# Optimization experiments

Hardware: AMD Instinct MI355X
Metric: run time of the kernel (lower is better)

The kernel has to match this reference:

```python
import jax, jax.numpy as jnp
import numpy as np

BATCH = 16384
IN_F = 4096
OUT_F = 4096
CP_H = 4
CP_W = 4
CP_B = 4


def _cubic_interp_matrix(n_out: int, n_cp: int, a: float = -0.75) -> jnp.ndarray:
    """Dense (n_out, n_cp) matrix replicating torch bicubic interpolation
    (Keys cubic convolution, a=-0.75) along one axis with align_corners=True
    and border replication (index clamping)."""
    # source coordinate for each output index (align_corners=True)
    x = jnp.arange(n_out, dtype=jnp.float32) * ((n_cp - 1) / (n_out - 1))
    x0 = jnp.floor(x)
    t = x - x0                      # fractional offset in [0,1)
    x0i = x0.astype(jnp.int32)

    def cub_inner(s):   # |s| <= 1
        return ((a + 2.0) * s - (a + 3.0)) * s * s + 1.0

    def cub_outer(s):   # 1 < |s| < 2
        return ((a * s - 5.0 * a) * s + 8.0 * a) * s - 4.0 * a

    # weights for taps at offsets -1, 0, +1, +2
    ws = (cub_outer(t + 1.0), cub_inner(t), cub_inner(1.0 - t), cub_outer(2.0 - t))
    A = jnp.zeros((n_out, n_cp), dtype=jnp.float32)
    for k, w in enumerate(ws):
        idx = jnp.clip(x0i + (k - 1), 0, n_cp - 1)  # replicate border
        A = A + w[:, None] * jax.nn.one_hot(idx, n_cp, dtype=jnp.float32)
    return A


def _linear_interp_matrix(n_out: int, n_cp: int) -> jnp.ndarray:
    """Dense (n_out, n_cp) matrix replicating torch 1-D linear interpolation
    with align_corners=True."""
    x = jnp.arange(n_out, dtype=jnp.float32) * ((n_cp - 1) / (n_out - 1))
    lo = jnp.floor(x).astype(jnp.int32)
    t = x - lo.astype(jnp.float32)
    hi = jnp.clip(lo + 1, 0, n_cp - 1)
    oh = lambda i: jax.nn.one_hot(i, n_cp, dtype=jnp.float32)
    return (1.0 - t)[:, None] * oh(lo) + t[:, None] * oh(hi)


def setup_inputs() -> dict:
    key = jax.random.key(0)
    k1, k2, k3 = jax.random.split(key, 3)
    return {
        "x": jax.random.normal(k1, (BATCH, IN_F), dtype=jnp.float32),
        "weight_cp": jax.random.normal(k2, (CP_H, CP_W), dtype=jnp.float32) * 0.02,
        "bias_cp": jax.random.normal(k3, (CP_B,), dtype=jnp.float32) * 0.02,
    }


def reference(x, weight_cp, bias_cp):
    # Bicubic-interpolated dense weight: W = A_out @ CP @ A_in^T  (out, in)
    A_out = _cubic_interp_matrix(OUT_F, CP_H)
    A_in = _cubic_interp_matrix(IN_F, CP_W)
    W = A_out @ weight_cp @ A_in.T
    # Linearly interpolated bias (out,)
    bias = _linear_interp_matrix(OUT_F, CP_B) @ bias_cp
    # F.linear: y = x @ W^T + b
    return x @ W.T + bias
```

## Files before the change

kernel.cpp:

```cpp
#include <hip/hip_runtime.h>
#include <cstddef>

#define BATCH 16384
#define IN_F  4096
#define OUT_F 4096
#define ROWS_PER_BLOCK 4
#define NBLOCKS (BATCH / ROWS_PER_BLOCK)

__device__ __forceinline__ float cub_inner(float s) {
    return (1.25f * s - 2.25f) * s * s + 1.0f;
}
__device__ __forceinline__ float cub_outer(float s) {
    return ((-0.75f * s + 3.75f) * s - 6.0f) * s + 3.0f;
}

__device__ __forceinline__ void cubic_row(int i, float& a0, float& a1, float& a2, float& a3) {
    const float inv = 3.0f / 4095.0f;
    const float xi = (float)i * inv;
    const float x0 = floorf(xi);
    const float t  = xi - x0;
    const int   c  = (int)x0;
    const float w0 = cub_outer(t + 1.0f);
    const float w1 = cub_inner(t);
    const float w2 = cub_inner(1.0f - t);
    const float w3 = cub_outer(2.0f - t);
    if (c == 0)      { a0 = w0 + w1; a1 = w2;   a2 = w3;   a3 = 0.0f; }
    else if (c == 1) { a0 = w0;      a1 = w1;   a2 = w2;   a3 = w3; }
    else if (c == 2) { a0 = 0.0f;    a1 = w0;   a2 = w1;   a3 = w2 + w3; }
    else             { a0 = 0.0f;    a1 = 0.0f; a2 = w0;   a3 = w1 + w2 + w3; }
}

__global__ __launch_bounds__(256) void k_init(const float* __restrict__ cp,
                                              const float* __restrict__ bcp,
                                              float4* __restrict__ Atab,
                                              float4* __restrict__ Mtab,
                                              float*  __restrict__ btab) {
    const int i = blockIdx.x * 256 + threadIdx.x;
    float a0, a1, a2, a3;
    cubic_row(i, a0, a1, a2, a3);
    Atab[i] = make_float4(a0, a1, a2, a3);

    float4 m;
    m.x = a0 * cp[0] + a1 * cp[4] + a2 * cp[8]  + a3 * cp[12];
    m.y = a0 * cp[1] + a1 * cp[5] + a2 * cp[9]  + a3 * cp[13];
    m.z = a0 * cp[2] + a1 * cp[6] + a2 * cp[10] + a3 * cp[14];
    m.w = a0 * cp[3] + a1 * cp[7] + a2 * cp[11] + a3 * cp[15];
    Mtab[i] = m;

    const float xb = (float)i * (3.0f / 4095.0f);
    const float lo = floorf(xb);
    const float tb = xb - lo;
    const int   l  = (int)lo;
    const float b0 = bcp[0], b1 = bcp[1], b2 = bcp[2], b3 = bcp[3];
    const float blo = (l == 0) ? b0 : (l == 1) ? b1 : (l == 2) ? b2 : b3;
    const float bhi = (l >= 2) ? b3 : (l == 1) ? b2 : b1;
    btab[i] = (1.0f - tb) * blo + tb * bhi;
}

__global__ __launch_bounds__(256) void k_fused(const float* __restrict__ x,
                                               const float4* __restrict__ Atab,
                                               const float4* __restrict__ Mtab,
                                               const float4* __restrict__ btabv,
                                               float* __restrict__ y) {
    const int tid  = threadIdx.x;
    const int wid  = tid >> 6;
    const int lane = tid & 63;
    const int row0 = blockIdx.x * ROWS_PER_BLOCK;

    __shared__ float4 part[4][ROWS_PER_BLOCK];

    float4 Af[16];
#pragma unroll
    for (int k = 0; k < 4; ++k)
#pragma unroll
        for (int j = 0; j < 4; ++j)
            Af[k * 4 + j] = Atab[1024 * k + 4 * tid + j];

    float4 acc[ROWS_PER_BLOCK];
#pragma unroll
    for (int r = 0; r < ROWS_PER_BLOCK; ++r) {
        const float4* xr = (const float4*)(x + (size_t)(row0 + r) * IN_F);
        float s0 = 0.f, s1 = 0.f, s2 = 0.f, s3 = 0.f;
#pragma unroll
        for (int k = 0; k < 4; ++k) {
            const float4 xv = xr[k * 256 + tid];
            const float4 A0 = Af[k * 4 + 0], A1 = Af[k * 4 + 1];
            const float4 A2 = Af[k * 4 + 2], A3 = Af[k * 4 + 3];
            s0 += A0.x * xv.x + A1.x * xv.y + A2.x * xv.z + A3.x * xv.w;
            s1 += A0.y * xv.x + A1.y * xv.y + A2.y * xv.z + A3.y * xv.w;
            s2 += A0.z * xv.x + A1.z * xv.y + A2.z * xv.z + A3.z * xv.w;
            s3 += A0.w * xv.x + A1.w * xv.y + A2.w * xv.z + A3.w * xv.w;
        }
        acc[r] = make_float4(s0, s1, s2, s3);
    }

#pragma unroll
    for (int off = 32; off > 0; off >>= 1) {
#pragma unroll
        for (int r = 0; r < ROWS_PER_BLOCK; ++r) {
            acc[r].x += __shfl_down(acc[r].x, off);
            acc[r].y += __shfl_down(acc[r].y, off);
            acc[r].z += __shfl_down(acc[r].z, off);
            acc[r].w += __shfl_down(acc[r].w, off);
        }
    }
    if (lane == 0) {
#pragma unroll
        for (int r = 0; r < ROWS_PER_BLOCK; ++r) part[wid][r] = acc[r];
    }
    __syncthreads();
    __builtin_amdgcn_sched_barrier(0);

    float4 Mf[16];
    float4 bf[4];
#pragma unroll
    for (int k = 0; k < 4; ++k) {
#pragma unroll
        for (int j = 0; j < 4; ++j)
            Mf[k * 4 + j] = Mtab[1024 * k + 4 * tid + j];
        bf[k] = btabv[256 * k + tid];
    }

#pragma unroll
    for (int r = 0; r < ROWS_PER_BLOCK; ++r) {
        const float4 p0 = part[0][r], p1 = part[1][r], p2 = part[2][r], p3 = part[3][r];
        float4 u;
        u.x = (p0.x + p1.x) + (p2.x + p3.x);
        u.y = (p0.y + p1.y) + (p2.y + p3.y);
        u.z = (p0.z + p1.z) + (p2.z + p3.z);
        u.w = (p0.w + p1.w) + (p2.w + p3.w);
        float4* yr = (float4*)(y + (size_t)(row0 + r) * OUT_F);
#pragma unroll
        for (int k = 0; k < 4; ++k) {
            const float4 M0 = Mf[k * 4 + 0], M1 = Mf[k * 4 + 1];
            const float4 M2 = Mf[k * 4 + 2], M3 = Mf[k * 4 + 3];
            float4 o;
            o.x = bf[k].x + M0.x * u.x + M0.y * u.y + M0.z * u.z + M0.w * u.w;
            o.y = bf[k].y + M1.x * u.x + M1.y * u.y + M1.z * u.z + M1.w * u.w;
            o.z = bf[k].z + M2.x * u.x + M2.y * u.y + M2.z * u.z + M2.w * u.w;
            o.w = bf[k].w + M3.x * u.x + M3.y * u.y + M3.z * u.z + M3.w * u.w;
            yr[k * 256 + tid] = o;
        }
    }
}

extern "C" void kernel_launch(void* const* d_in, const int* in_sizes, int n_in,
                              void* d_out, int out_size, void* d_ws, size_t ws_size,
                              hipStream_t stream) {
    const float* x   = (const float*)d_in[0];
    const float* cp  = (const float*)d_in[1];
    const float* bcp = (const float*)d_in[2];
    float* y = (float*)d_out;

    float4* Atab = (float4*)d_ws;
    float4* Mtab = (float4*)((char*)d_ws + 64 * 1024);
    float*  btab = (float*)((char*)d_ws + 128 * 1024);

    k_init<<<dim3(IN_F / 256), dim3(256), 0, stream>>>(cp, bcp, Atab, Mtab, btab);
    k_fused<<<dim3(NBLOCKS), dim3(256), 0, stream>>>(x, Atab, Mtab, (const float4*)btab, y);
}
```

Before: 455.7 us.

## Warp-specialize fused kernel into producer and consumer halves with double-buffered partials

Splits each 512-thread block into four producer waves that reduce x rows against the A table and four consumer waves that expand and write y. Partial sums pass through a double-buffered shared array, and each block now handles 32 rows in 8 groups. This is meant to overlap the read of x with the write of y and to load the A, M and bias tables once per 32 rows instead of once per 4. In exchange it adds a block barrier per group and leaves half the threads idle in each phase. The kernel was already bandwidth-bound, so the gain may be limited.

Measured after the change: 447.6 us. Within noise of the previous version (-1.8%).

```diff
diff --git a/kernel.cpp b/kernel.cpp
--- a/kernel.cpp
+++ b/kernel.cpp
@@ -4,7 +4,9 @@
 #define BATCH 16384
 #define IN_F  4096
 #define OUT_F 4096
-#define ROWS_PER_BLOCK 4
+#define RPG    4
+#define GROUPS 8
+#define ROWS_PER_BLOCK (RPG * GROUPS)
 #define NBLOCKS (BATCH / ROWS_PER_BLOCK)
 
 __device__ __forceinline__ float cub_inner(float s) {
@@ -57,7 +59,7 @@
     btab[i] = (1.0f - tb) * blo + tb * bhi;
 }
 
-__global__ __launch_bounds__(256) void k_fused(const float* __restrict__ x,
+__global__ __launch_bounds__(512) void k_fused(const float* __restrict__ x,
                                                const float4* __restrict__ Atab,
                                                const float4* __restrict__ Mtab,
                                                const float4* __restrict__ btabv,
@@ -67,79 +69,94 @@
     const int lane = tid & 63;
     const int row0 = blockIdx.x * ROWS_PER_BLOCK;
 
-    __shared__ float4 part[4][ROWS_PER_BLOCK];
+    __shared__ float4 part[2][RPG][4];
 
-    float4 Af[16];
+    if (wid < 4) {
+        const int p = tid;
+        float4 Af[16];
 #pragma unroll
-    for (int k = 0; k < 4; ++k)
+        for (int k = 0; k < 4; ++k)
 #pragma unroll
-        for (int j = 0; j < 4; ++j)
-            Af[k * 4 + j] = Atab[1024 * k + 4 * tid + j];
+            for (int j = 0; j < 4; ++j)
+                Af[k * 4 + j] = Atab[1024 * k + 4 * p + j];
 
-    float4 acc[ROWS_PER_BLOCK];
+        auto produce = [&](int g) {
+            const float* xg = x + (size_t)(row0 + g * RPG) * IN_F;
+            float4 acc[RPG];
 #pragma unroll
-    for (int r = 0; r < ROWS_PER_BLOCK; ++r) {
-        const float4* xr = (const float4*)(x + (size_t)(row0 + r) * IN_F);
-        float s0 = 0.f, s1 = 0.f, s2 = 0.f, s3 = 0.f;
+            for (int r = 0; r < RPG; ++r) {
+                const float4* xr = (const float4*)(xg + (size_t)r * IN_F);
+                float s0 = 0.f, s1 = 0.f, s2 = 0.f, s3 = 0.f;
+#pragma unroll
+                for (int k = 0; k < 4; ++k) {
+                    const float4 xv = xr[k * 256 + p];
+                    const float4 A0 = Af[k * 4 + 0], A1 = Af[k * 4 + 1];
+                    const float4 A2 = Af[k * 4 + 2], A3 = Af[k * 4 + 3];
+                    s0 += A0.x * xv.x + A1.x * xv.y + A2.x * xv.z + A3.x * xv.w;
+                    s1 += A0.y * xv.x + A1.y * xv.y + A2.y * xv.z + A3.y * xv.w;
+                    s2 += A0.z * xv.x + A1.z * xv.y + A2.z * xv.z + A3.z * xv.w;
+                    s3 += A0.w * xv.x + A1.w * xv.y + A2.w * xv.z + A3.w * xv.w;
+                }
+                acc[r] = make_float4(s0, s1, s2, s3);
+            }
+#pragma unroll
+            for (int off = 32; off > 0; off >>= 1)
+#pragma unroll
+                for (int r = 0; r < RPG; ++r) {
+                    acc[r].x += __shfl_down(acc[r].x, off);
+                    acc[r].y += __shfl_down(acc[r].y, off);
+                    acc[r].z += __shfl_down(acc[r].z, off);
+                    acc[r].w += __shfl_down(acc[r].w, off);
+                }
+            if (lane == 0) {
+#pragma unroll
+                for (int r = 0; r < RPG; ++r) part[g & 1][r][wid] = acc[r];
+            }
+        };
+
+        produce(0);
+        __syncthreads();
+        for (int g = 0; g < GROUPS; ++g) {
+            if (g + 1 < GROUPS) produce(g + 1);
+            __syncthreads();
+        }
+    } else {
+        const int c = tid - 256;
+        float4 Mf[16];
+        float4 bf[4];
 #pragma unroll
         for (int k = 0; k < 4; ++k) {
-            const float4 xv = xr[k * 256 + tid];
-            const float4 A0 = Af[k * 4 + 0], A1 = Af[k * 4 + 1];
-            const float4 A2 = Af[k * 4 + 2], A3 = Af[k * 4 + 3];
-            s0 += A0.x * xv.x + A1.x * xv.y + A2.x * xv.z + A3.x * xv.w;
-            s1 += A0.y * xv.x + A1.y * xv.y + A2.y * xv.z + A3.y * xv.w;
-            s2 += A0.z * xv.x + A1.z * xv.y + A2.z * xv.z + A3.z * xv.w;
-            s3 += A0.w * xv.x + A1.w * xv.y + A2.w * xv.z + A3.w * xv.w;
+#pragma unroll
+            for (int j = 0; j < 4; ++j)
+                Mf[k * 4 + j] = Mtab[1024 * k + 4 * c + j];
+            bf[k] = btabv[256 * k + c];
         }
-        acc[r] = make_float4(s0, s1, s2, s3);
-    }
 
+        __syncthreads();
+        for (int g = 0; g < GROUPS; ++g) {
 #pragma unroll
-    for (int off = 32; off > 0; off >>= 1) {
+            for (int r = 0; r < RPG; ++r) {
+                const float4 p0 = part[g & 1][r][0], p1 = part[g & 1][r][1];
+                const float4 p2 = part[g & 1][r][2], p3 = part[g & 1][r][3];
+                float4 u;
+                u.x = (p0.x + p1.x) + (p2.x + p3.x);
+                u.y = (p0.y + p1.y) + (p2.y + p3.y);
+                u.z = (p0.z + p1.z) + (p2.z + p3.z);
+                u.w = (p0.w + p1.w) + (p2.w + p3.w);
+                float4* yr = (float4*)(y + (size_t)(row0 + g * RPG + r) * OUT_F);
 #pragma unroll
-        for (int r = 0; r < ROWS_PER_BLOCK; ++r) {
-            acc[r].x += __shfl_down(acc[r].x, off);
-            acc[r].y += __shfl_down(acc[r].y, off);
-            acc[r].z += __shfl_down(acc[r].z, off);
-            acc[r].w += __shfl_down(acc[r].w, off);
-        }
-    }
-    if (lane == 0) {
-#pragma unroll
-        for (int r = 0; r < ROWS_PER_BLOCK; ++r) part[wid][r] = acc[r];
-    }
-    __syncthreads();
-    __builtin_amdgcn_sched_barrier(0);
-
-    float4 Mf[16];
-    float4 bf[4];
-#pragma unroll
-    for (int k = 0; k < 4; ++k) {
-#pragma unroll
-        for (int j = 0; j < 4; ++j)
-            Mf[k * 4 + j] = Mtab[1024 * k + 4 * tid + j];
-        bf[k] = btabv[256 * k + tid];
-    }
-
-#pragma unroll
-    for (int r = 0; r < ROWS_PER_BLOCK; ++r) {
-        const float4 p0 = part[0][r], p1 = part[1][r], p2 = part[2][r], p3 = part[3][r];
-        float4 u;
-        u.x = (p0.x + p1.x) + (p2.x + p3.x);
-        u.y = (p0.y + p1.y) + (p2.y + p3.y);
-        u.z = (p0.z + p1.z) + (p2.z + p3.z);
-        u.w = (p0.w + p1.w) + (p2.w + p3.w);
-        float4* yr = (float4*)(y + (size_t)(row0 + r) * OUT_F);
-#pragma unroll
-        for (int k = 0; k < 4; ++k) {
-            const float4 M0 = Mf[k * 4 + 0], M1 = Mf[k * 4 + 1];
-            const float4 M2 = Mf[k * 4 + 2], M3 = Mf[k * 4 + 3];
-            float4 o;
-            o.x = bf[k].x + M0.x * u.x + M0.y * u.y + M0.z * u.z + M0.w * u.w;
-            o.y = bf[k].y + M1.x * u.x + M1.y * u.y + M1.z * u.z + M1.w * u.w;
-            o.z = bf[k].z + M2.x * u.x + M2.y * u.y + M2.z * u.z + M2.w * u.w;
-            o.w = bf[k].w + M3.x * u.x + M3.y * u.y + M3.z * u.z + M3.w * u.w;
-            yr[k * 256 + tid] = o;
+                for (int k = 0; k < 4; ++k) {
+                    const float4 M0 = Mf[k * 4 + 0], M1 = Mf[k * 4 + 1];
+                    const float4 M2 = Mf[k * 4 + 2], M3 = Mf[k * 4 + 3];
+                    float4 o;
+                    o.x = bf[k].x + M0.x * u.x + M0.y * u.y + M0.z * u.z + M0.w * u.w;
+                    o.y = bf[k].y + M1.x * u.x + M1.y * u.y + M1.z * u.z + M1.w * u.w;
+                    o.z = bf[k].z + M2.x * u.x + M2.y * u.y + M2.z * u.z + M2.w * u.w;
+                    o.w = bf[k].w + M3.x * u.x + M3.y * u.y + M3.z * u.z + M3.w * u.w;
+                    yr[k * 256 + c] = o;
+                }
+            }
+            __syncthreads();
         }
     }
 }
@@ -157,5 +174,5 @@
     float*  btab = (float*)((char*)d_ws + 128 * 1024);
 
     k_init<<<dim3(IN_F / 256), dim3(256), 0, stream>>>(cp, bcp, Atab, Mtab, btab);
-    k_fused<<<dim3(NBLOCKS), dim3(256), 0, stream>>>(x, Atab, Mtab, (const float4*)btab, y);
+    k_fused<<<dim3(NBLOCKS), dim3(512), 0, stream>>>(x, Atab, Mtab, (const float4*)btab, y);
 }
```
